# Performance work log

Measured on AMD Instinct MI355X. Metric: run time of the kernel, lower is better.

## Reference

```python
import jax, jax.numpy as jnp
import numpy as np

EPS = 1e-12  # torch F.normalize eps

def l2norm(x, axis=-1):
    n = jnp.linalg.norm(x, axis=axis, keepdims=True)
    return x / jnp.maximum(n, EPS)

def setup_inputs() -> dict:
    key = jax.random.key(0)
    ks = jax.random.split(key, 8)
    n_vocab, d, n_asp = 100000, 256, 14
    B, L, M = 512, 100, 10
    pos = jax.random.randint(ks[0], (B, L), 0, n_vocab)
    negs = jax.random.randint(ks[1], (B, M, L), 0, n_vocab)
    E_w = jax.random.normal(ks[2], (n_vocab, d), dtype=jnp.float32) * 0.1
    T_w = jax.random.normal(ks[3], (n_asp, d), dtype=jnp.float32) * 0.1
    M_w = jax.random.uniform(ks[4], (d, d), dtype=jnp.float32, minval=-0.1, maxval=0.1)
    M_b = jnp.zeros((d,), dtype=jnp.float32)
    lin_w = jax.random.normal(ks[5], (n_asp, d), dtype=jnp.float32) * 0.05
    lin_b = jnp.zeros((n_asp,), dtype=jnp.float32)
    return {"pos": pos, "negs": negs, "E_w": E_w, "T_w": T_w,
            "M_w": M_w, "M_b": M_b, "lin_w": lin_w, "lin_b": lin_b}

def reference(pos, negs, E_w, T_w, M_w, M_b, lin_w, lin_b):
    # e: [B, L, d] (original keeps e_i as [B, d, L]; layout differs, math identical)
    e = E_w[pos]
    y_s = jnp.mean(e, axis=1)                    # mean over tokens -> [B, d]
    My = y_s @ M_w.T + M_b                       # [B, d]
    d_i = jnp.tanh(jnp.einsum('bld,bd->bl', e, My))  # [B, L]
    # NOTE: original normalizes exp(d_i) by the GLOBAL sum over the whole batch
    a_i = jnp.exp(d_i) / jnp.sum(jnp.exp(d_i))   # [B, L]
    z_s = l2norm(jnp.einsum('bld,bl->bd', e, a_i))   # [B, d]
    p_t = jax.nn.softmax(z_s @ lin_w.T + lin_b, axis=1)  # [B, n_asp]
    r_s = l2norm(p_t @ T_w)                      # [B, d]
    e_n = E_w[negs]                              # [B, M, L, d]
    z_n = l2norm(jnp.mean(e_n, axis=2))          # [B, M, d]
    return (r_s, z_s, z_n)
```

## Files before the change

### kernel.cpp

```cpp
#include <hip/hip_runtime.h>
#include <math.h>

#define D 256

__device__ __forceinline__ float wave_reduce_sum(float v) {
#pragma unroll
    for (int off = 32; off > 0; off >>= 1) v += __shfl_xor(v, off);
    return v;
}
__device__ __forceinline__ float wave_reduce_max(float v) {
#pragma unroll
    for (int off = 32; off > 0; off >>= 1) v = fmaxf(v, __shfl_xor(v, off));
    return v;
}

__device__ __forceinline__ float4 load_row_f32(const float* __restrict__ E_w,
                                               int idx, int lane) {
    return ((const float4*)(E_w + (size_t)idx * D))[lane];
}
__device__ __forceinline__ float4 load_row_i8(const signed char* __restrict__ Eq,
                                              const float* __restrict__ scales,
                                              int idx, int lane) {
    const char4 c = ((const char4*)(Eq + (size_t)idx * D))[lane];
    const float f = scales[idx];
    return make_float4(f * (float)c.x, f * (float)c.y,
                       f * (float)c.z, f * (float)c.w);
}
template <bool I8>
__device__ __forceinline__ float4 load_row(const float* __restrict__ E_w,
                                           const signed char* __restrict__ Eq,
                                           const float* __restrict__ scales,
                                           int idx, int lane) {
    return I8 ? load_row_i8(Eq, scales, idx, lane) : load_row_f32(E_w, idx, lane);
}

template <int NB>
__device__ __forceinline__ void gather_batch_i8(
    const signed char* __restrict__ Eq, const float* __restrict__ scales,
    const int* __restrict__ idxp, int l, int lane, float4& acc) {
    int id[NB];
#pragma unroll
    for (int k = 0; k < NB; ++k) id[k] = idxp[l + k];
    char4 c[NB];
#pragma unroll
    for (int k = 0; k < NB; ++k)
        c[k] = ((const char4*)(Eq + (size_t)id[k] * D))[lane];
    float f[NB];
#pragma unroll
    for (int k = 0; k < NB; ++k) f[k] = scales[id[k]];
#pragma unroll
    for (int k = 0; k < NB; ++k) {
        acc.x += f[k] * (float)c[k].x;
        acc.y += f[k] * (float)c[k].y;
        acc.z += f[k] * (float)c[k].z;
        acc.w += f[k] * (float)c[k].w;
    }
}

__global__ __launch_bounds__(256) void convert_i8_kernel(
    const float* __restrict__ E_w, signed char* __restrict__ Eq,
    float* __restrict__ scales, int n_vocab) {
    const int lane = threadIdx.x & 63;
    const int gw   = (blockIdx.x * 256 + threadIdx.x) >> 6;
    const int nw   = (gridDim.x * 256) >> 6;

    for (int r0 = gw * 4; r0 < n_vocab; r0 += nw * 4) {
        const int n = min(4, n_vocab - r0);
        float4 v[4];
#pragma unroll
        for (int k = 0; k < 4; ++k)
            if (k < n) v[k] = load_row_f32(E_w, r0 + k, lane);
#pragma unroll
        for (int k = 0; k < 4; ++k) {
            if (k >= n) break;
            float mx = fmaxf(fmaxf(fabsf(v[k].x), fabsf(v[k].y)),
                             fmaxf(fabsf(v[k].z), fabsf(v[k].w)));
            mx = wave_reduce_max(mx);
            const float inv = (mx > 0.f) ? 127.f / mx : 0.f;
            const int qx = __float2int_rn(v[k].x * inv);
            const int qy = __float2int_rn(v[k].y * inv);
            const int qz = __float2int_rn(v[k].z * inv);
            const int qw = __float2int_rn(v[k].w * inv);
            const unsigned int packed =
                ((unsigned int)(unsigned char)(signed char)qx) |
                ((unsigned int)(unsigned char)(signed char)qy << 8) |
                ((unsigned int)(unsigned char)(signed char)qz << 16) |
                ((unsigned int)(unsigned char)(signed char)qw << 24);
            ((unsigned int*)(Eq + (size_t)(r0 + k) * D))[lane] = packed;
            if (lane == 0) scales[r0 + k] = mx * (1.f / 127.f);
        }
    }
}

template <bool I8>
__global__ __launch_bounds__(256) void abae_fused_kernel(
    const int* __restrict__ pos, const int* __restrict__ negs,
    const float* __restrict__ E_w, const signed char* __restrict__ Eq,
    const float* __restrict__ scales, const float* __restrict__ T_w,
    const float* __restrict__ M_w, const float* __restrict__ M_b,
    const float* __restrict__ lin_w, const float* __restrict__ lin_b,
    float* __restrict__ r_s, float* __restrict__ z_s, float* __restrict__ z_n,
    int B, int BM, int L, int n_asp) {
    const int t    = threadIdx.x;
    const int lane = t & 63;
    const int wv   = t >> 6;

    __shared__ float4 sred[4][64];
    __shared__ float  sy[D];
    __shared__ float  smy[D];
    __shared__ float  slog[16];
    __shared__ float  sp[16];
    __shared__ float  sscal[4];

    const int C = (L + 3) / 4;

    if (blockIdx.x < (unsigned)BM) {
        const int bm = blockIdx.x;
        const int* __restrict__ idxp = negs + (size_t)bm * L;
        const int s0 = wv * C;
        const int e0 = min(L, s0 + C);

        float4 acc = make_float4(0.f, 0.f, 0.f, 0.f);
        int l = s0;
        if (I8) {
            for (; l + 13 <= e0; l += 13) gather_batch_i8<13>(Eq, scales, idxp, l, lane, acc);
            for (; l + 6 <= e0; l += 6)   gather_batch_i8<6>(Eq, scales, idxp, l, lane, acc);
            for (; l < e0; ++l) {
                const float4 v = load_row_i8(Eq, scales, idxp[l], lane);
                acc.x += v.x; acc.y += v.y; acc.z += v.z; acc.w += v.w;
            }
        } else {
            for (; l < e0; ++l) {
                const float4 v = load_row_f32(E_w, idxp[l], lane);
                acc.x += v.x; acc.y += v.y; acc.z += v.z; acc.w += v.w;
            }
        }
        sred[wv][lane] = acc;
        __syncthreads();
        if (wv == 0) {
            float4 z  = sred[0][lane];
            const float4 a1 = sred[1][lane], a2 = sred[2][lane], a3 = sred[3][lane];
            const float invL = 1.f / (float)L;
            z.x = (z.x + a1.x + a2.x + a3.x) * invL;
            z.y = (z.y + a1.y + a2.y + a3.y) * invL;
            z.z = (z.z + a1.z + a2.z + a3.z) * invL;
            z.w = (z.w + a1.w + a2.w + a3.w) * invL;
            float ss = z.x * z.x + z.y * z.y + z.z * z.z + z.w * z.w;
            ss = wave_reduce_sum(ss);
            const float inv = 1.f / fmaxf(sqrtf(ss), 1e-12f);
            z.x *= inv; z.y *= inv; z.z *= inv; z.w *= inv;
            ((float4*)(z_n + (size_t)bm * D))[lane] = z;
        }
        return;
    }

    const int b = blockIdx.x - BM;
    const int* __restrict__ posb = pos + (size_t)b * L;
    const int s0 = wv * C;
    const int e0 = min(L, s0 + C);

    float4 acc = make_float4(0.f, 0.f, 0.f, 0.f);
    int l = s0;
    if (I8) {
        for (; l + 13 <= e0; l += 13) gather_batch_i8<13>(Eq, scales, posb, l, lane, acc);
        for (; l + 6 <= e0; l += 6)   gather_batch_i8<6>(Eq, scales, posb, l, lane, acc);
    }
    for (; l < e0; ++l) {
        const float4 v = load_row<I8>(E_w, Eq, scales, posb[l], lane);
        acc.x += v.x; acc.y += v.y; acc.z += v.z; acc.w += v.w;
    }
    sred[wv][lane] = acc;
    __syncthreads();
    if (wv == 0) {
        float4 y  = sred[0][lane];
        const float4 a1 = sred[1][lane], a2 = sred[2][lane], a3 = sred[3][lane];
        const float invL = 1.f / (float)L;
        y.x = (y.x + a1.x + a2.x + a3.x) * invL;
        y.y = (y.y + a1.y + a2.y + a3.y) * invL;
        y.z = (y.z + a1.z + a2.z + a3.z) * invL;
        y.w = (y.w + a1.w + a2.w + a3.w) * invL;
        ((float4*)sy)[lane] = y;
    }
    __syncthreads();

    {
        const float4 y4 = ((const float4*)sy)[lane];
        for (int r0 = wv * 64; r0 < wv * 64 + 64; r0 += 4) {
            const float4 m0 = ((const float4*)(M_w + (size_t)(r0 + 0) * D))[lane];
            const float4 m1 = ((const float4*)(M_w + (size_t)(r0 + 1) * D))[lane];
            const float4 m2 = ((const float4*)(M_w + (size_t)(r0 + 2) * D))[lane];
            const float4 m3 = ((const float4*)(M_w + (size_t)(r0 + 3) * D))[lane];
            float p0 = m0.x * y4.x + m0.y * y4.y + m0.z * y4.z + m0.w * y4.w;
            float p1 = m1.x * y4.x + m1.y * y4.y + m1.z * y4.z + m1.w * y4.w;
            float p2 = m2.x * y4.x + m2.y * y4.y + m2.z * y4.z + m2.w * y4.w;
            float p3 = m3.x * y4.x + m3.y * y4.y + m3.z * y4.z + m3.w * y4.w;
#pragma unroll
            for (int off = 32; off > 0; off >>= 1) {
                p0 += __shfl_xor(p0, off);
                p1 += __shfl_xor(p1, off);
                p2 += __shfl_xor(p2, off);
                p3 += __shfl_xor(p3, off);
            }
            if (lane == 0) {
                smy[r0 + 0] = p0 + M_b[r0 + 0];
                smy[r0 + 1] = p1 + M_b[r0 + 1];
                smy[r0 + 2] = p2 + M_b[r0 + 2];
                smy[r0 + 3] = p3 + M_b[r0 + 3];
            }
        }
    }
    __syncthreads();

    const float4 my4 = ((const float4*)smy)[lane];
    float4 zacc = make_float4(0.f, 0.f, 0.f, 0.f);
    l = s0;
    for (; l + 1 < e0; l += 2) {
        const float4 ea = load_row<I8>(E_w, Eq, scales, posb[l], lane);
        const float4 eb = load_row<I8>(E_w, Eq, scales, posb[l + 1], lane);
        float pa = ea.x * my4.x + ea.y * my4.y + ea.z * my4.z + ea.w * my4.w;
        float pb = eb.x * my4.x + eb.y * my4.y + eb.z * my4.z + eb.w * my4.w;
#pragma unroll
        for (int off = 32; off > 0; off >>= 1) {
            pa += __shfl_xor(pa, off);
            pb += __shfl_xor(pb, off);
        }
        const float wa = expf(tanhf(pa));
        const float wb = expf(tanhf(pb));
        zacc.x += ea.x * wa + eb.x * wb;
        zacc.y += ea.y * wa + eb.y * wb;
        zacc.z += ea.z * wa + eb.z * wb;
        zacc.w += ea.w * wa + eb.w * wb;
    }
    for (; l < e0; ++l) {
        const float4 ea = load_row<I8>(E_w, Eq, scales, posb[l], lane);
        float pa = ea.x * my4.x + ea.y * my4.y + ea.z * my4.z + ea.w * my4.w;
        pa = wave_reduce_sum(pa);
        const float wa = expf(tanhf(pa));
        zacc.x += ea.x * wa; zacc.y += ea.y * wa;
        zacc.z += ea.z * wa; zacc.w += ea.w * wa;
    }
    sred[wv][lane] = zacc;
    __syncthreads();
    if (wv == 0) {
        float4 z  = sred[0][lane];
        const float4 a1 = sred[1][lane], a2 = sred[2][lane], a3 = sred[3][lane];
        z.x += a1.x + a2.x + a3.x;
        z.y += a1.y + a2.y + a3.y;
        z.z += a1.z + a2.z + a3.z;
        z.w += a1.w + a2.w + a3.w;
        float ss = z.x * z.x + z.y * z.y + z.z * z.z + z.w * z.w;
        ss = wave_reduce_sum(ss);
        const float inv = 1.f / fmaxf(sqrtf(ss), 1e-12f);
        z.x *= inv; z.y *= inv; z.z *= inv; z.w *= inv;
        ((float4*)(z_s + (size_t)b * D))[lane] = z;
        ((float4*)sy)[lane] = z;
    }
    __syncthreads();

    const float4 z4 = ((const float4*)sy)[lane];
    for (int a = wv; a < n_asp; a += 4) {
        const float4 w4 = ((const float4*)(lin_w + (size_t)a * D))[lane];
        float p = z4.x * w4.x + z4.y * w4.y + z4.z * w4.z + z4.w * w4.w;
        p = wave_reduce_sum(p);
        if (lane == 0) slog[a] = p + lin_b[a];
    }
    __syncthreads();
    if (t == 0) {
        float mx = -1e30f;
        for (int a = 0; a < n_asp; ++a) mx = fmaxf(mx, slog[a]);
        float s = 0.f;
        for (int a = 0; a < n_asp; ++a) {
            const float e = expf(slog[a] - mx);
            sp[a] = e; s += e;
        }
        const float invs = 1.f / s;
        for (int a = 0; a < n_asp; ++a) sp[a] *= invs;
    }
    __syncthreads();

    float r = 0.f;
    for (int a = 0; a < n_asp; ++a) r += sp[a] * T_w[(size_t)a * D + t];
    const float sq = wave_reduce_sum(r * r);
    if (lane == 0) sscal[wv] = sq;
    __syncthreads();
    const float tot = sscal[0] + sscal[1] + sscal[2] + sscal[3];
    const float inv = 1.f / fmaxf(sqrtf(tot), 1e-12f);
    r_s[(size_t)b * D + t] = r * inv;
}

extern "C" void kernel_launch(void* const* d_in, const int* in_sizes, int n_in,
                              void* d_out, int out_size, void* d_ws, size_t ws_size,
                              hipStream_t stream) {
    const int*   pos   = (const int*)d_in[0];
    const int*   negs  = (const int*)d_in[1];
    const float* E_w   = (const float*)d_in[2];
    const float* T_w   = (const float*)d_in[3];
    const float* M_w   = (const float*)d_in[4];
    const float* M_b   = (const float*)d_in[5];
    const float* lin_w = (const float*)d_in[6];
    const float* lin_b = (const float*)d_in[7];
    float* out = (float*)d_out;

    const int d       = in_sizes[5];
    const int n_asp   = in_sizes[7];
    const int M       = in_sizes[1] / in_sizes[0];
    const int B       = out_size / (d * (2 + M));
    const int L       = in_sizes[0] / B;
    const int n_vocab = in_sizes[2] / d;
    (void)n_in;

    float* r_s = out;
    float* z_s = out + (size_t)B * d;
    float* z_n = out + (size_t)2 * B * d;

    const int BM = B * M;

    const size_t need = (size_t)n_vocab * D + (size_t)n_vocab * sizeof(float);
    const bool use_i8 = ws_size >= need;

    signed char* Eq = (signed char*)d_ws;
    float* scales   = (float*)(Eq + (size_t)n_vocab * D);

    if (use_i8) {
        convert_i8_kernel<<<2048, 256, 0, stream>>>(E_w, Eq, scales, n_vocab);
        abae_fused_kernel<true><<<BM + B, 256, 0, stream>>>(
            pos, negs, E_w, Eq, scales, T_w, M_w, M_b, lin_w, lin_b,
            r_s, z_s, z_n, B, BM, L, n_asp);
    } else {
        abae_fused_kernel<false><<<BM + B, 256, 0, stream>>>(
            pos, negs, E_w, (const signed char*)nullptr, (const float*)nullptr,
            T_w, M_w, M_b, lin_w, lin_b, r_s, z_s, z_n, B, BM, L, n_asp);
    }
}
```

Before: 224.4 us.

## Batch eight positive rows per block to amortize M_w reads and barriers

Positive-sample blocks now handle eight batch rows each, two per wave, and are launched ahead of the negative-sample blocks. The M_w matrix-vector product is computed for all eight rows together, so each M_w row is read once per block instead of once per batch row. The attention, softmax and r_s stages run per wave, which removes most block-level syncs and shared-memory reductions. The int8 gather batch size also changes to 5. The cost is far fewer, longer-running positive blocks, with each wave walking the full sequence serially, which could lengthen the critical path.

```diff
diff --git a/kernel.cpp b/kernel.cpp
--- a/kernel.cpp
+++ b/kernel.cpp
@@ -55,6 +55,10 @@
         acc.z += f[k] * (float)c[k].z;
         acc.w += f[k] * (float)c[k].w;
     }
+}
+
+__device__ __forceinline__ float dot4(const float4 a, const float4 b) {
+    return a.x * b.x + a.y * b.y + a.z * b.z + a.w * b.w;
 }
 
 __global__ __launch_bounds__(256) void convert_i8_kernel(
@@ -100,31 +104,27 @@
     const float* __restrict__ M_w, const float* __restrict__ M_b,
     const float* __restrict__ lin_w, const float* __restrict__ lin_b,
     float* __restrict__ r_s, float* __restrict__ z_s, float* __restrict__ z_n,
-    int B, int BM, int L, int n_asp) {
+    int B, int BM, int nmain, int L, int n_asp) {
     const int t    = threadIdx.x;
     const int lane = t & 63;
     const int wv   = t >> 6;
 
-    __shared__ float4 sred[4][64];
-    __shared__ float  sy[D];
-    __shared__ float  smy[D];
-    __shared__ float  slog[16];
-    __shared__ float  sp[16];
-    __shared__ float  sscal[4];
-
-    const int C = (L + 3) / 4;
-
-    if (blockIdx.x < (unsigned)BM) {
-        const int bm = blockIdx.x;
+    __shared__ float4 syy[8][64];
+    __shared__ float  smy[8][256];
+    __shared__ float  slog[4][2][16];
+
+    if (blockIdx.x >= (unsigned)nmain) {
+        const int bm = blockIdx.x - nmain;
         const int* __restrict__ idxp = negs + (size_t)bm * L;
+        const int C  = (L + 3) / 4;
         const int s0 = wv * C;
         const int e0 = min(L, s0 + C);
 
         float4 acc = make_float4(0.f, 0.f, 0.f, 0.f);
         int l = s0;
         if (I8) {
-            for (; l + 13 <= e0; l += 13) gather_batch_i8<13>(Eq, scales, idxp, l, lane, acc);
-            for (; l + 6 <= e0; l += 6)   gather_batch_i8<6>(Eq, scales, idxp, l, lane, acc);
+            for (; l + 5 <= e0; l += 5)
+                gather_batch_i8<5>(Eq, scales, idxp, l, lane, acc);
             for (; l < e0; ++l) {
                 const float4 v = load_row_i8(Eq, scales, idxp[l], lane);
                 acc.x += v.x; acc.y += v.y; acc.z += v.z; acc.w += v.w;
@@ -135,17 +135,17 @@
                 acc.x += v.x; acc.y += v.y; acc.z += v.z; acc.w += v.w;
             }
         }
-        sred[wv][lane] = acc;
+        syy[wv][lane] = acc;
         __syncthreads();
         if (wv == 0) {
-            float4 z  = sred[0][lane];
-            const float4 a1 = sred[1][lane], a2 = sred[2][lane], a3 = sred[3][lane];
+            float4 z  = syy[0][lane];
+            const float4 a1 = syy[1][lane], a2 = syy[2][lane], a3 = syy[3][lane];
             const float invL = 1.f / (float)L;
             z.x = (z.x + a1.x + a2.x + a3.x) * invL;
             z.y = (z.y + a1.y + a2.y + a3.y) * invL;
             z.z = (z.z + a1.z + a2.z + a3.z) * invL;
             z.w = (z.w + a1.w + a2.w + a3.w) * invL;
-            float ss = z.x * z.x + z.y * z.y + z.z * z.z + z.w * z.w;
+            float ss = dot4(z, z);
             ss = wave_reduce_sum(ss);
             const float inv = 1.f / fmaxf(sqrtf(ss), 1e-12f);
             z.x *= inv; z.y *= inv; z.z *= inv; z.w *= inv;
@@ -154,138 +154,163 @@
         return;
     }
 
-    const int b = blockIdx.x - BM;
-    const int* __restrict__ posb = pos + (size_t)b * L;
-    const int s0 = wv * C;
-    const int e0 = min(L, s0 + C);
-
-    float4 acc = make_float4(0.f, 0.f, 0.f, 0.f);
-    int l = s0;
-    if (I8) {
-        for (; l + 13 <= e0; l += 13) gather_batch_i8<13>(Eq, scales, posb, l, lane, acc);
-        for (; l + 6 <= e0; l += 6)   gather_batch_i8<6>(Eq, scales, posb, l, lane, acc);
-    }
-    for (; l < e0; ++l) {
-        const float4 v = load_row<I8>(E_w, Eq, scales, posb[l], lane);
-        acc.x += v.x; acc.y += v.y; acc.z += v.z; acc.w += v.w;
-    }
-    sred[wv][lane] = acc;
+    const int b0 = blockIdx.x * 8;
+    const int bj0 = b0 + wv * 2;
+    const float invL = 1.f / (float)L;
+
+#pragma unroll
+    for (int j = 0; j < 2; ++j) {
+        const int b = bj0 + j;
+        float4 acc = make_float4(0.f, 0.f, 0.f, 0.f);
+        if (b < B) {
+            const int* __restrict__ posb = pos + (size_t)b * L;
+            int l = 0;
+            if (I8) {
+                for (; l + 5 <= L; l += 5)
+                    gather_batch_i8<5>(Eq, scales, posb, l, lane, acc);
+            }
+            for (; l < L; ++l) {
+                const float4 v = load_row<I8>(E_w, Eq, scales, posb[l], lane);
+                acc.x += v.x; acc.y += v.y; acc.z += v.z; acc.w += v.w;
+            }
+        }
+        acc.x *= invL; acc.y *= invL; acc.z *= invL; acc.w *= invL;
+        syy[wv * 2 + j][lane] = acc;
+    }
     __syncthreads();
-    if (wv == 0) {
-        float4 y  = sred[0][lane];
-        const float4 a1 = sred[1][lane], a2 = sred[2][lane], a3 = sred[3][lane];
-        const float invL = 1.f / (float)L;
-        y.x = (y.x + a1.x + a2.x + a3.x) * invL;
-        y.y = (y.y + a1.y + a2.y + a3.y) * invL;
-        y.z = (y.z + a1.z + a2.z + a3.z) * invL;
-        y.w = (y.w + a1.w + a2.w + a3.w) * invL;
-        ((float4*)sy)[lane] = y;
+
+    for (int r = wv * 64; r < wv * 64 + 64; r += 2) {
+        const float4 m0 = ((const float4*)(M_w + (size_t)(r + 0) * D))[lane];
+        const float4 m1 = ((const float4*)(M_w + (size_t)(r + 1) * D))[lane];
+        float p[16];
+#pragma unroll
+        for (int bb = 0; bb < 8; ++bb) {
+            const float4 y = syy[bb][lane];
+            p[bb]     = dot4(m0, y);
+            p[8 + bb] = dot4(m1, y);
+        }
+#pragma unroll
+        for (int off = 32; off > 0; off >>= 1) {
+#pragma unroll
+            for (int k = 0; k < 16; ++k) p[k] += __shfl_xor(p[k], off);
+        }
+        if (lane == 0) {
+            const float mb0 = M_b[r], mb1 = M_b[r + 1];
+#pragma unroll
+            for (int bb = 0; bb < 8; ++bb) {
+                smy[bb][r]     = p[bb] + mb0;
+                smy[bb][r + 1] = p[8 + bb] + mb1;
+            }
+        }
     }
     __syncthreads();
 
+    float4 my[2], zq[2];
+#pragma unroll
+    for (int j = 0; j < 2; ++j) {
+        my[j] = ((const float4*)smy[wv * 2 + j])[lane];
+        zq[j] = make_float4(0.f, 0.f, 0.f, 0.f);
+    }
     {
-        const float4 y4 = ((const float4*)sy)[lane];
-        for (int r0 = wv * 64; r0 < wv * 64 + 64; r0 += 4) {
-            const float4 m0 = ((const float4*)(M_w + (size_t)(r0 + 0) * D))[lane];
-            const float4 m1 = ((const float4*)(M_w + (size_t)(r0 + 1) * D))[lane];
-            const float4 m2 = ((const float4*)(M_w + (size_t)(r0 + 2) * D))[lane];
-            const float4 m3 = ((const float4*)(M_w + (size_t)(r0 + 3) * D))[lane];
-            float p0 = m0.x * y4.x + m0.y * y4.y + m0.z * y4.z + m0.w * y4.w;
-            float p1 = m1.x * y4.x + m1.y * y4.y + m1.z * y4.z + m1.w * y4.w;
-            float p2 = m2.x * y4.x + m2.y * y4.y + m2.z * y4.z + m2.w * y4.w;
-            float p3 = m3.x * y4.x + m3.y * y4.y + m3.z * y4.z + m3.w * y4.w;
+        const int bA = bj0, bB = bj0 + 1;
+        const bool okA = bA < B, okB = bB < B;
+        const int* __restrict__ pA = pos + (size_t)(okA ? bA : 0) * L;
+        const int* __restrict__ pB = pos + (size_t)(okB ? bB : 0) * L;
+        int l = 0;
+        for (; l + 2 <= L; l += 2) {
+            const float4 e00 = load_row<I8>(E_w, Eq, scales, pA[l], lane);
+            const float4 e01 = load_row<I8>(E_w, Eq, scales, pA[l + 1], lane);
+            const float4 e10 = load_row<I8>(E_w, Eq, scales, pB[l], lane);
+            const float4 e11 = load_row<I8>(E_w, Eq, scales, pB[l + 1], lane);
+            float p00 = dot4(e00, my[0]), p01 = dot4(e01, my[0]);
+            float p10 = dot4(e10, my[1]), p11 = dot4(e11, my[1]);
+#pragma unroll
+            for (int off = 32; off > 0; off >>= 1) {
+                p00 += __shfl_xor(p00, off);
+                p01 += __shfl_xor(p01, off);
+                p10 += __shfl_xor(p10, off);
+                p11 += __shfl_xor(p11, off);
+            }
+            const float w00 = expf(tanhf(p00)), w01 = expf(tanhf(p01));
+            const float w10 = expf(tanhf(p10)), w11 = expf(tanhf(p11));
+            zq[0].x += e00.x * w00 + e01.x * w01;
+            zq[0].y += e00.y * w00 + e01.y * w01;
+            zq[0].z += e00.z * w00 + e01.z * w01;
+            zq[0].w += e00.w * w00 + e01.w * w01;
+            zq[1].x += e10.x * w10 + e11.x * w11;
+            zq[1].y += e10.y * w10 + e11.y * w11;
+            zq[1].z += e10.z * w10 + e11.z * w11;
+            zq[1].w += e10.w * w10 + e11.w * w11;
+        }
+        for (; l < L; ++l) {
+            const float4 e0 = load_row<I8>(E_w, Eq, scales, pA[l], lane);
+            const float4 e1 = load_row<I8>(E_w, Eq, scales, pB[l], lane);
+            float p0 = dot4(e0, my[0]), p1 = dot4(e1, my[1]);
 #pragma unroll
             for (int off = 32; off > 0; off >>= 1) {
                 p0 += __shfl_xor(p0, off);
                 p1 += __shfl_xor(p1, off);
-                p2 += __shfl_xor(p2, off);
-                p3 += __shfl_xor(p3, off);
-            }
-            if (lane == 0) {
-                smy[r0 + 0] = p0 + M_b[r0 + 0];
-                smy[r0 + 1] = p1 + M_b[r0 + 1];
-                smy[r0 + 2] = p2 + M_b[r0 + 2];
-                smy[r0 + 3] = p3 + M_b[r0 + 3];
-            }
-        }
-    }
-    __syncthreads();
-
-    const float4 my4 = ((const float4*)smy)[lane];
-    float4 zacc = make_float4(0.f, 0.f, 0.f, 0.f);
-    l = s0;
-    for (; l + 1 < e0; l += 2) {
-        const float4 ea = load_row<I8>(E_w, Eq, scales, posb[l], lane);
-        const float4 eb = load_row<I8>(E_w, Eq, scales, posb[l + 1], lane);
-        float pa = ea.x * my4.x + ea.y * my4.y + ea.z * my4.z + ea.w * my4.w;
-        float pb = eb.x * my4.x + eb.y * my4.y + eb.z * my4.z + eb.w * my4.w;
+            }
+            const float w0 = expf(tanhf(p0)), w1 = expf(tanhf(p1));
+            zq[0].x += e0.x * w0; zq[0].y += e0.y * w0;
+            zq[0].z += e0.z * w0; zq[0].w += e0.w * w0;
+            zq[1].x += e1.x * w1; zq[1].y += e1.y * w1;
+            zq[1].z += e1.z * w1; zq[1].w += e1.w * w1;
+        }
+    }
+#pragma unroll
+    for (int j = 0; j < 2; ++j) {
+        float ss = wave_reduce_sum(dot4(zq[j], zq[j]));
+        const float inv = 1.f / fmaxf(sqrtf(ss), 1e-12f);
+        zq[j].x *= inv; zq[j].y *= inv; zq[j].z *= inv; zq[j].w *= inv;
+        const int b = bj0 + j;
+        if (b < B) ((float4*)(z_s + (size_t)b * D))[lane] = zq[j];
+    }
+
+    for (int a = 0; a < n_asp; ++a) {
+        const float4 w4 = ((const float4*)(lin_w + (size_t)a * D))[lane];
+        float p0 = dot4(zq[0], w4);
+        float p1 = dot4(zq[1], w4);
 #pragma unroll
         for (int off = 32; off > 0; off >>= 1) {
-            pa += __shfl_xor(pa, off);
-            pb += __shfl_xor(pb, off);
-        }
-        const float wa = expf(tanhf(pa));
-        const float wb = expf(tanhf(pb));
-        zacc.x += ea.x * wa + eb.x * wb;
-        zacc.y += ea.y * wa + eb.y * wb;
-        zacc.z += ea.z * wa + eb.z * wb;
-        zacc.w += ea.w * wa + eb.w * wb;
-    }
-    for (; l < e0; ++l) {
-        const float4 ea = load_row<I8>(E_w, Eq, scales, posb[l], lane);
-        float pa = ea.x * my4.x + ea.y * my4.y + ea.z * my4.z + ea.w * my4.w;
-        pa = wave_reduce_sum(pa);
-        const float wa = expf(tanhf(pa));
-        zacc.x += ea.x * wa; zacc.y += ea.y * wa;
-        zacc.z += ea.z * wa; zacc.w += ea.w * wa;
-    }
-    sred[wv][lane] = zacc;
-    __syncthreads();
-    if (wv == 0) {
-        float4 z  = sred[0][lane];
-        const float4 a1 = sred[1][lane], a2 = sred[2][lane], a3 = sred[3][lane];
-        z.x += a1.x + a2.x + a3.x;
-        z.y += a1.y + a2.y + a3.y;
-        z.z += a1.z + a2.z + a3.z;
-        z.w += a1.w + a2.w + a3.w;
-        float ss = z.x * z.x + z.y * z.y + z.z * z.z + z.w * z.w;
-        ss = wave_reduce_sum(ss);
-        const float inv = 1.f / fmaxf(sqrtf(ss), 1e-12f);
-        z.x *= inv; z.y *= inv; z.z *= inv; z.w *= inv;
-        ((float4*)(z_s + (size_t)b * D))[lane] = z;
-        ((float4*)sy)[lane] = z;
-    }
-    __syncthreads();
-
-    const float4 z4 = ((const float4*)sy)[lane];
-    for (int a = wv; a < n_asp; a += 4) {
-        const float4 w4 = ((const float4*)(lin_w + (size_t)a * D))[lane];
-        float p = z4.x * w4.x + z4.y * w4.y + z4.z * w4.z + z4.w * w4.w;
-        p = wave_reduce_sum(p);
-        if (lane == 0) slog[a] = p + lin_b[a];
-    }
-    __syncthreads();
-    if (t == 0) {
-        float mx = -1e30f;
-        for (int a = 0; a < n_asp; ++a) mx = fmaxf(mx, slog[a]);
-        float s = 0.f;
-        for (int a = 0; a < n_asp; ++a) {
-            const float e = expf(slog[a] - mx);
-            sp[a] = e; s += e;
-        }
-        const float invs = 1.f / s;
-        for (int a = 0; a < n_asp; ++a) sp[a] *= invs;
-    }
-    __syncthreads();
-
-    float r = 0.f;
-    for (int a = 0; a < n_asp; ++a) r += sp[a] * T_w[(size_t)a * D + t];
-    const float sq = wave_reduce_sum(r * r);
-    if (lane == 0) sscal[wv] = sq;
-    __syncthreads();
-    const float tot = sscal[0] + sscal[1] + sscal[2] + sscal[3];
-    const float inv = 1.f / fmaxf(sqrtf(tot), 1e-12f);
-    r_s[(size_t)b * D + t] = r * inv;
+            p0 += __shfl_xor(p0, off);
+            p1 += __shfl_xor(p1, off);
+        }
+        if (lane == 0) {
+            const float lb = lin_b[a];
+            slog[wv][0][a] = p0 + lb;
+            slog[wv][1][a] = p1 + lb;
+        }
+    }
+    float mx[2] = {-1e30f, -1e30f}, sum[2] = {0.f, 0.f};
+#pragma unroll
+    for (int j = 0; j < 2; ++j) {
+        for (int a = 0; a < n_asp; ++a) mx[j] = fmaxf(mx[j], slog[wv][j][a]);
+        for (int a = 0; a < n_asp; ++a) sum[j] += expf(slog[wv][j][a] - mx[j]);
+        sum[j] = 1.f / sum[j];
+    }
+
+    float4 r0 = make_float4(0.f, 0.f, 0.f, 0.f);
+    float4 r1 = make_float4(0.f, 0.f, 0.f, 0.f);
+    for (int a = 0; a < n_asp; ++a) {
+        const float4 t4 = ((const float4*)(T_w + (size_t)a * D))[lane];
+        const float pa0 = expf(slog[wv][0][a] - mx[0]) * sum[0];
+        const float pa1 = expf(slog[wv][1][a] - mx[1]) * sum[1];
+        r0.x += pa0 * t4.x; r0.y += pa0 * t4.y;
+        r0.z += pa0 * t4.z; r0.w += pa0 * t4.w;
+        r1.x += pa1 * t4.x; r1.y += pa1 * t4.y;
+        r1.z += pa1 * t4.z; r1.w += pa1 * t4.w;
+    }
+    {
+        float ss0 = wave_reduce_sum(dot4(r0, r0));
+        float ss1 = wave_reduce_sum(dot4(r1, r1));
+        const float i0 = 1.f / fmaxf(sqrtf(ss0), 1e-12f);
+        const float i1 = 1.f / fmaxf(sqrtf(ss1), 1e-12f);
+        r0.x *= i0; r0.y *= i0; r0.z *= i0; r0.w *= i0;
+        r1.x *= i1; r1.y *= i1; r1.z *= i1; r1.w *= i1;
+        if (bj0 < B)     ((float4*)(r_s + (size_t)bj0 * D))[lane] = r0;
+        if (bj0 + 1 < B) ((float4*)(r_s + (size_t)(bj0 + 1) * D))[lane] = r1;
+    }
 }
 
 extern "C" void kernel_launch(void* const* d_in, const int* in_sizes, int n_in,
@@ -313,7 +338,8 @@
     float* z_s = out + (size_t)B * d;
     float* z_n = out + (size_t)2 * B * d;
 
-    const int BM = B * M;
+    const int BM    = B * M;
+    const int nmain = (B + 7) / 8;
 
     const size_t need = (size_t)n_vocab * D + (size_t)n_vocab * sizeof(float);
     const bool use_i8 = ws_size >= need;
@@ -323,12 +349,12 @@
 
     if (use_i8) {
         convert_i8_kernel<<<2048, 256, 0, stream>>>(E_w, Eq, scales, n_vocab);
-        abae_fused_kernel<true><<<BM + B, 256, 0, stream>>>(
+        abae_fused_kernel<true><<<nmain + BM, 256, 0, stream>>>(
             pos, negs, E_w, Eq, scales, T_w, M_w, M_b, lin_w, lin_b,
-            r_s, z_s, z_n, B, BM, L, n_asp);
+            r_s, z_s, z_n, B, BM, nmain, L, n_asp);
     } else {
-        abae_fused_kernel<false><<<BM + B, 256, 0, stream>>>(
+        abae_fused_kernel<false><<<nmain + BM, 256, 0, stream>>>(
             pos, negs, E_w, (const signed char*)nullptr, (const float*)nullptr,
-            T_w, M_w, M_b, lin_w, lin_b, r_s, z_s, z_n, B, BM, L, n_asp);
-    }
-}
+            T_w, M_w, M_b, lin_w, lin_b, r_s, z_s, z_n, B, BM, nmain, L, n_asp);
+    }
+}
```

New measurement: 310.0 us. 1.38x slower.
